# Optimization experiments

Measured on AMD Instinct MI355X. Metric: run time of the kernel, lower is better.

## Reference

```python
import jax, jax.numpy as jnp
import numpy as np

N_NODES = 100000
N_EDGES = 800000
N_GRAPHS = 64
D = 256
IN_FEAT = 59
MLP_DIMS = [D // 2, D // 2, D // 4, D // 8, 1]  # 128->128->64->32->1


def _glorot(key, shape):
    fan_in = shape[0] if len(shape) > 1 else shape[0]
    return jax.random.normal(key, shape, dtype=jnp.float32) / jnp.sqrt(jnp.float32(fan_in))


def setup_inputs() -> dict:
    key = jax.random.key(0)
    ks = list(jax.random.split(key, 40))
    inp = {}
    inp['x'] = jax.random.normal(ks[0], (N_NODES, IN_FEAT), dtype=jnp.float32)
    inp['edge_index'] = jax.random.randint(ks[1], (2, N_EDGES), 0, N_NODES, dtype=jnp.int64 if jax.config.jax_enable_x64 else jnp.int32)
    inp['batch'] = jnp.sort(jax.random.randint(ks[2], (N_NODES,), 0, N_GRAPHS, dtype=jnp.int32))
    # GATConv params (heads=1): lin weight, att_src, att_dst, bias
    dims = [(IN_FEAT, D), (D, D // 2), (D // 2, D // 2)]
    ki = 3
    for li, (di, do) in enumerate(dims, start=1):
        inp[f'W{li}'] = _glorot(ks[ki], (di, do)); ki += 1
        inp[f'as{li}'] = _glorot(ks[ki], (do,)); ki += 1
        inp[f'ad{li}'] = _glorot(ks[ki], (do,)); ki += 1
        inp[f'b{li}'] = jnp.zeros((do,), dtype=jnp.float32)
    # policy / value MLPs
    for pre in ('p', 'v'):
        for j in range(4):
            inp[f'{pre}W{j}'] = _glorot(ks[ki], (MLP_DIMS[j], MLP_DIMS[j + 1])); ki += 1
            inp[f'{pre}b{j}'] = jnp.zeros((MLP_DIMS[j + 1],), dtype=jnp.float32)
    return inp


def gat_conv(x, src, dst, W, a_src, a_dst, b, n_nodes):
    """PyG GATConv, heads=1, self-loops already included in src/dst."""
    h = x @ W  # [N, Do]
    s = h @ a_src  # [N] per-node source score
    d = h @ a_dst  # [N] per-node target score
    e = jax.nn.leaky_relu(s[src] + d[dst], negative_slope=0.2)  # [E]
    m = jax.ops.segment_max(e, dst, num_segments=n_nodes)
    m = jnp.where(jnp.isfinite(m), m, 0.0)
    ex = jnp.exp(e - m[dst])
    den = jax.ops.segment_sum(ex, dst, num_segments=n_nodes)
    alpha = ex / (den[dst] + 1e-16)  # edge softmax over incoming edges
    out = jax.ops.segment_sum(h[src] * alpha[:, None], dst, num_segments=n_nodes)
    return out + b


def mlp(h, Ws, bs):
    # hidden layers with ReLU, final layer linear
    for W, b in zip(Ws[:-1], bs[:-1]):
        h = jax.nn.relu(h @ W + b)
    return h @ Ws[-1] + bs[-1]


def reference(x, edge_index, batch,
              W1, as1, ad1, b1, W2, as2, ad2, b2, W3, as3, ad3, b3,
              pW0, pb0, pW1, pb1, pW2, pb2, pW3, pb3,
              vW0, vb0, vW1, vb1, vW2, vb2, vW3, vb3):
    n = x.shape[0]
    loop = jnp.arange(n, dtype=edge_index.dtype)
    src = jnp.concatenate([edge_index[0], loop])  # PyG adds self-loops
    dst = jnp.concatenate([edge_index[1], loop])
    out = jax.nn.relu(gat_conv(x, src, dst, W1, as1, ad1, b1, n))
    out = jax.nn.relu(gat_conv(out, src, dst, W2, as2, ad2, b2, n))
    out = jax.nn.relu(gat_conv(out, src, dst, W3, as3, ad3, b3, n))
    policy = mlp(out, [pW0, pW1, pW2, pW3], [pb0, pb1, pb2, pb3])  # [N, 1]
    pooled = jax.ops.segment_sum(out, batch, num_segments=N_GRAPHS)  # global_add_pool
    value = mlp(pooled, [vW0, vW1, vW2, vW3], [vb0, vb1, vb2, vb3])  # [G, 1]
    # Original returns policy split per-graph (data-dependent slicing); the
    # dense [N,1] policy plus batch ids carries the same information.
    return policy, value
```

## Files before the change

kernel.cpp:

```cpp
#include <hip/hip_runtime.h>
#include <hip/hip_bf16.h>
#include <cstdint>

#define N_NODES 100000
#define N_EDGES 800000
#define N_GRAPHS 64
#define POOL_SPLIT 16

typedef short short8 __attribute__((ext_vector_type(8)));
typedef float f32x4 __attribute__((ext_vector_type(4)));

__device__ __forceinline__ float leakyf(float x){ return x >= 0.0f ? x : 0.2f*x; }
__device__ __forceinline__ float reluf(float x){ return x > 0.0f ? x : 0.0f; }

__device__ __forceinline__ float bf2f(unsigned short u){
  union { uint32_t i; float f; } c; c.i = ((uint32_t)u) << 16; return c.f;
}
__device__ __forceinline__ unsigned short f2bf(float x){
  union { float f; uint32_t i; } c; c.f = x;
  uint32_t r = c.i + 0x7FFFu + ((c.i >> 16) & 1u);
  return (unsigned short)(r >> 16);
}
__device__ __forceinline__ uint32_t pack2(float a, float b){
  return (uint32_t)f2bf(a) | ((uint32_t)f2bf(b) << 16);
}

__global__ __launch_bounds__(256) void x2bf_kernel(const float* __restrict__ x,
    uint32_t* __restrict__ xb, int n){
  int idx = blockIdx.x*256 + threadIdx.x;
  if (idx >= n*32) return;
  int v = idx >> 5, c2 = (idx & 31)*2;
  float f0 = (c2   < 59) ? x[(size_t)v*59 + c2]     : 0.f;
  float f1 = (c2+1 < 59) ? x[(size_t)v*59 + c2 + 1] : 0.f;
  xb[idx] = pack2(f0, f1);
}

__global__ void zero_deg_kernel(int* __restrict__ deg, int n){
  int v = blockIdx.x*256 + threadIdx.x;
  if (v < n) deg[v] = 0;
}
__global__ void count_kernel(const int* __restrict__ dst, int* __restrict__ deg,
                             int* __restrict__ pos, int E){
  int e = blockIdx.x*256 + threadIdx.x;
  if (e < E) pos[e] = atomicAdd(&deg[dst[e]], 1);
}
__global__ __launch_bounds__(256) void scan1_kernel(const int* __restrict__ deg,
    int* __restrict__ rowptr, int* __restrict__ bsum, int n){
  __shared__ int sm[256];
  int t = threadIdx.x, i = blockIdx.x*256 + t;
  int v = (i < n) ? deg[i] : 0;
  sm[t] = v; __syncthreads();
  for (int off = 1; off < 256; off <<= 1){
    int x = (t >= off) ? sm[t-off] : 0;
    __syncthreads();
    sm[t] += x;
    __syncthreads();
  }
  if (i < n) rowptr[i] = sm[t] - v;
  if (t == 255) bsum[blockIdx.x] = sm[255];
}
__global__ __launch_bounds__(512) void scan2_kernel(int* __restrict__ bsum, int nb){
  __shared__ int sm[512];
  int t = threadIdx.x;
  int v = (t < nb) ? bsum[t] : 0;
  sm[t] = v; __syncthreads();
  for (int off = 1; off < 512; off <<= 1){
    int x = (t >= off) ? sm[t-off] : 0;
    __syncthreads();
    sm[t] += x;
    __syncthreads();
  }
  if (t < nb) bsum[t] = sm[t] - v;
}
__global__ void scan3_kernel(int* __restrict__ rowptr, const int* __restrict__ bsum, int n){
  int i = blockIdx.x*256 + threadIdx.x;
  if (i < n) rowptr[i] += bsum[blockIdx.x];
}
__global__ void scatter_kernel(const int* __restrict__ src, const int* __restrict__ dst,
                               const int* __restrict__ rowptr, const int* __restrict__ pos,
                               int* __restrict__ csr, int E){
  int e = blockIdx.x*256 + threadIdx.x;
  if (e < E) csr[rowptr[dst[e]] + pos[e]] = src[e];
}

__global__ __launch_bounds__(256) void wa_all_kernel(
    const float* __restrict__ W1, const float* __restrict__ as1, const float* __restrict__ ad1,
    const float* __restrict__ W2, const float* __restrict__ as2, const float* __restrict__ ad2,
    const float* __restrict__ W3, const float* __restrict__ as3, const float* __restrict__ ad3,
    float* __restrict__ wa){
  int t = threadIdx.x;
  { float ss=0.f, dd=0.f; const float* wr = W2 + (size_t)t*128;
    for (int o=0;o<128;++o){ float w=wr[o]; ss+=w*as2[o]; dd+=w*ad2[o]; }
    wa[128+t]=ss; wa[384+t]=dd; }
  if (t < 128){ float ss=0.f, dd=0.f; const float* wr = W3 + (size_t)t*128;
    for (int o=0;o<128;++o){ float w=wr[o]; ss+=w*as3[o]; dd+=w*ad3[o]; }
    wa[640+t]=ss; wa[768+t]=dd; }
  if (t < 64){ float ss=0.f, dd=0.f;
    if (t < 59){ const float* wr = W1 + (size_t)t*256;
      for (int o=0;o<256;++o){ float w=wr[o]; ss+=w*as1[o]; dd+=w*ad1[o]; } }
    wa[t]=ss; wa[64+t]=dd; }
}

__global__ __launch_bounds__(256) void sd_bf16_kernel(const unsigned short* __restrict__ in,
    const float* __restrict__ wa_s, const float* __restrict__ wa_d,
    float* __restrict__ s, float* __restrict__ d, int n, int K){
  int wid = threadIdx.x >> 6, lane = threadIdx.x & 63;
  int v = (blockIdx.x << 2) + wid;
  if (v >= n) return;
  float ss = 0.f, dd = 0.f;
  const unsigned short* row = in + (size_t)v*K;
  for (int k = lane*2; k < K; k += 128){
    uint32_t u = *(const uint32_t*)&row[k];
    float x0 = bf2f((unsigned short)(u & 0xFFFFu));
    float x1 = bf2f((unsigned short)(u >> 16));
    ss += x0*wa_s[k] + x1*wa_s[k+1];
    dd += x0*wa_d[k] + x1*wa_d[k+1];
  }
  for (int off = 32; off; off >>= 1){ ss += __shfl_down(ss, off); dd += __shfl_down(dd, off); }
  if (lane == 0){ s[v] = ss; d[v] = dd; }
}

template<int NC>
__device__ __forceinline__ void gload(const unsigned short* rowp, int hl, float* f){
  if constexpr (NC == 1){
    uint32_t u = ((const uint32_t*)rowp)[hl];
    f[0] = bf2f((unsigned short)(u & 0xFFFFu));
    f[1] = bf2f((unsigned short)(u >> 16));
  } else {
    uint2 u = ((const uint2*)rowp)[hl];
    f[0] = bf2f((unsigned short)(u.x & 0xFFFFu));
    f[1] = bf2f((unsigned short)(u.x >> 16));
    f[2] = bf2f((unsigned short)(u.y & 0xFFFFu));
    f[3] = bf2f((unsigned short)(u.y >> 16));
  }
}

template<int NC, int BR>
__global__ __launch_bounds__(256) void agg_half(
    const unsigned short* __restrict__ hb, const float* __restrict__ s,
    const float* __restrict__ dsc, const int* __restrict__ rowptr,
    const int* __restrict__ deg, const int* __restrict__ csr, float* __restrict__ ew,
    const float* __restrict__ bias, unsigned short* __restrict__ outp, int n){
  const int C = NC*64;
  const int tid = threadIdx.x;
  const int hl   = tid & 31;
  const int base = tid & 32;
  const int v = blockIdx.x*8 + (tid >> 5);
  if (v >= n) return;
  const int beg = rowptr[v], dg = deg[v];
  const float dv = dsc[v];
  const float e0 = leakyf(s[v] + dv);
  float acc[2*NC];

  if (dg <= 32){
    int srcl = 0; float sc = -1e30f;
    if (hl < dg){ srcl = csr[beg + hl]; sc = leakyf(s[srcl] + dv); }
    float mm = sc;
    #pragma unroll
    for (int off = 16; off; off >>= 1) mm = fmaxf(mm, __shfl_xor(mm, off));
    const float m = fmaxf(e0, mm);
    float w = (hl < dg) ? __expf(sc - m) : 0.f;
    float den = w;
    #pragma unroll
    for (int off = 16; off; off >>= 1) den += __shfl_xor(den, off);
    const float ws0 = __expf(e0 - m);
    const float inv = 1.0f / (den + ws0 + 1e-16f);
    const float wl = w * inv;
    {
      float f[2*NC]; gload<NC>(hb + (size_t)v*C, hl, f);
      const float w0 = ws0 * inv;
      #pragma unroll
      for (int c = 0; c < 2*NC; ++c) acc[c] = w0 * f[c];
    }
    int j = 0;
    for (; j + 4 <= dg; j += 4){
      int  s0 = __shfl(srcl, base+j),   s1 = __shfl(srcl, base+j+1);
      int  s2 = __shfl(srcl, base+j+2), s3 = __shfl(srcl, base+j+3);
      float w0_ = __shfl(wl, base+j),   w1_ = __shfl(wl, base+j+1);
      float w2_ = __shfl(wl, base+j+2), w3_ = __shfl(wl, base+j+3);
      float f0[2*NC], f1[2*NC], f2[2*NC], f3[2*NC];
      gload<NC>(hb + (size_t)s0*C, hl, f0);
      gload<NC>(hb + (size_t)s1*C, hl, f1);
      gload<NC>(hb + (size_t)s2*C, hl, f2);
      gload<NC>(hb + (size_t)s3*C, hl, f3);
      #pragma unroll
      for (int c = 0; c < 2*NC; ++c)
        acc[c] += w0_*f0[c] + w1_*f1[c] + w2_*f2[c] + w3_*f3[c];
    }
    for (; j < dg; ++j){
      int src = __shfl(srcl, base+j);
      float w_ = __shfl(wl, base+j);
      float f[2*NC]; gload<NC>(hb + (size_t)src*C, hl, f);
      #pragma unroll
      for (int c = 0; c < 2*NC; ++c) acc[c] += w_*f[c];
    }
  } else {
    float m = e0;
    for (int b0 = 0; b0 < dg; b0 += 32){
      int i = b0 + hl; float sc = -1e30f;
      if (i < dg){ int src = csr[beg + i]; sc = leakyf(s[src] + dv); ew[beg + i] = sc; }
      #pragma unroll
      for (int off = 16; off; off >>= 1) sc = fmaxf(sc, __shfl_xor(sc, off));
      m = fmaxf(m, sc);
    }
    float dsum = 0.f;
    for (int b0 = 0; b0 < dg; b0 += 32){
      int i = b0 + hl; float w = 0.f;
      if (i < dg){ w = __expf(ew[beg + i] - m); ew[beg + i] = w; }
      float cs = w;
      #pragma unroll
      for (int off = 16; off; off >>= 1) cs += __shfl_xor(cs, off);
      dsum += cs;
    }
    const float ws0 = __expf(e0 - m);
    const float inv = 1.0f / (dsum + ws0 + 1e-16f);
    {
      float f[2*NC]; gload<NC>(hb + (size_t)v*C, hl, f);
      const float w0 = ws0 * inv;
      #pragma unroll
      for (int c = 0; c < 2*NC; ++c) acc[c] = w0 * f[c];
    }
    for (int b0 = 0; b0 < dg; b0 += 32){
      int i = b0 + hl;
      int srcl = 0; float wl = 0.f;
      if (i < dg){ srcl = csr[beg + i]; wl = ew[beg + i] * inv; }
      int cnt = min(32, dg - b0);
      for (int j = 0; j < cnt; ++j){
        int src = __shfl(srcl, base+j);
        float w_ = __shfl(wl, base+j);
        float f[2*NC]; gload<NC>(hb + (size_t)src*C, hl, f);
        #pragma unroll
        for (int c = 0; c < 2*NC; ++c) acc[c] += w_*f[c];
      }
    }
  }

  unsigned short* op = outp + (size_t)v*C;
  if constexpr (NC == 1){
    float v0 = acc[0], v1 = acc[1];
    if constexpr (BR){ v0 = reluf(v0 + bias[2*hl]); v1 = reluf(v1 + bias[2*hl+1]); }
    ((uint32_t*)op)[hl] = pack2(v0, v1);
  } else {
    float v0=acc[0], v1=acc[1], v2=acc[2], v3=acc[3];
    if constexpr (BR){
      v0 = reluf(v0 + bias[4*hl]);   v1 = reluf(v1 + bias[4*hl+1]);
      v2 = reluf(v2 + bias[4*hl+2]); v3 = reluf(v3 + bias[4*hl+3]);
    }
    uint2 u; u.x = pack2(v0, v1); u.y = pack2(v2, v3);
    ((uint2*)op)[hl] = u;
  }
}

template<int ABF, int OBF>
__global__ __launch_bounds__(256) void gemm_mfma(
    const void* __restrict__ Av, const float* __restrict__ W,
    const float* __restrict__ bias, void* __restrict__ Cv,
    int M, int K, int Kw, int N, int act){
  __shared__ short As[64][40];
  __shared__ short Bs[64][40];
  const int t = threadIdx.x;
  const int row0 = blockIdx.x * 64;
  const int col0 = blockIdx.y * 64;
  const int wv = t >> 6, lane = t & 63;
  const int wr = wv >> 1, wc = wv & 1;
  const int lr = lane & 15, lg = lane >> 4;

  f32x4 acc00 = {}, acc01 = {}, acc10 = {}, acc11 = {};

  for (int k0 = 0; k0 < K; k0 += 32){
    {
      int m = t >> 2, kq = (t & 3) * 8;
      int gr = row0 + m;
      short8 av;
      if constexpr (ABF == 1){
        const unsigned short* Au = (const unsigned short*)Av;
        if (gr < M && (k0 + kq + 7) < K){
          av = *(const short8*)&Au[(size_t)gr*K + k0 + kq];
        } else {
          #pragma unroll
          for (int j = 0; j < 8; ++j){
            int gk = k0 + kq + j;
            av[j] = (gr < M && gk < K) ? (short)Au[(size_t)gr*K + gk] : (short)0;
          }
        }
      } else {
        const float* Af = (const float*)Av;
        if (gr < M && (K % 4) == 0 && (k0 + kq + 7) < K){
          const float4 f0 = *(const float4*)&Af[(size_t)gr*K + k0 + kq];
          const float4 f1 = *(const float4*)&Af[(size_t)gr*K + k0 + kq + 4];
          av[0]=f2bf(f0.x); av[1]=f2bf(f0.y); av[2]=f2bf(f0.z); av[3]=f2bf(f0.w);
          av[4]=f2bf(f1.x); av[5]=f2bf(f1.y); av[6]=f2bf(f1.z); av[7]=f2bf(f1.w);
        } else {
          #pragma unroll
          for (int j = 0; j < 8; ++j){
            int gk = k0 + kq + j;
            float val = (gr < M && gk < K) ? Af[(size_t)gr*K + gk] : 0.f;
            av[j] = f2bf(val);
          }
        }
      }
      *(short8*)&As[m][kq] = av;
    }
    {
      int n = t & 63, k8 = (t >> 6) * 8;
      short8 bv;
      #pragma unroll
      for (int j = 0; j < 8; ++j){
        int gk = k0 + k8 + j;
        float val = (gk < Kw) ? W[(size_t)gk*N + col0 + n] : 0.f;
        bv[j] = f2bf(val);
      }
      *(short8*)&Bs[n][k8] = bv;
    }
    __syncthreads();
    short8 af0 = *(short8*)&As[wr*32 +  0 + lr][lg*8];
    short8 af1 = *(short8*)&As[wr*32 + 16 + lr][lg*8];
    short8 bf0 = *(short8*)&Bs[wc*32 +  0 + lr][lg*8];
    short8 bf1 = *(short8*)&Bs[wc*32 + 16 + lr][lg*8];
    acc00 = __builtin_amdgcn_mfma_f32_16x16x32_bf16(af0, bf0, acc00, 0, 0, 0);
    acc01 = __builtin_amdgcn_mfma_f32_16x16x32_bf16(af0, bf1, acc01, 0, 0, 0);
    acc10 = __builtin_amdgcn_mfma_f32_16x16x32_bf16(af1, bf0, acc10, 0, 0, 0);
    acc11 = __builtin_amdgcn_mfma_f32_16x16x32_bf16(af1, bf1, acc11, 0, 0, 0);
    __syncthreads();
  }

  #pragma unroll
  for (int fm = 0; fm < 2; ++fm){
    #pragma unroll
    for (int fn = 0; fn < 2; ++fn){
      const f32x4 a = (fm==0) ? (fn==0 ? acc00 : acc01) : (fn==0 ? acc10 : acc11);
      int col = col0 + wc*32 + fn*16 + lr;
      float bv = bias ? bias[col] : 0.f;
      #pragma unroll
      for (int j = 0; j < 4; ++j){
        int row = row0 + wr*32 + fm*16 + lg*4 + j;
        if (row >= M) continue;
        float val = a[j] + bv;
        if (act) val = reluf(val);
        if constexpr (OBF == 0) ((float*)Cv)[(size_t)row*N + col] = val;
        else ((unsigned short*)Cv)[(size_t)row*N + col] = f2bf(val);
      }
    }
  }
}

__global__ __launch_bounds__(256) void policy_tail_kernel(
    const float* __restrict__ p2, const float* __restrict__ W2, const float* __restrict__ B2,
    const float* __restrict__ W3, const float* __restrict__ B3,
    float* __restrict__ out, int n){
  __shared__ float w2[64*32];
  __shared__ float w3[32];
  __shared__ float b2s[32];
  int t = threadIdx.x;
  for (int i = t; i < 2048; i += 256) w2[i] = W2[i];
  if (t < 32){ w3[t] = W3[t]; b2s[t] = B2[t]; }
  __syncthreads();
  int v = blockIdx.x*256 + t;
  if (v >= n) return;
  const float* row = p2 + (size_t)v*64;
  float acc32[32];
  #pragma unroll
  for (int o = 0; o < 32; ++o) acc32[o] = b2s[o];
  for (int k = 0; k < 64; ++k){
    float xk = row[k];
    #pragma unroll
    for (int o = 0; o < 32; ++o) acc32[o] += xk * w2[k*32 + o];
  }
  float accf = B3[0];
  #pragma unroll
  for (int o = 0; o < 32; ++o) accf += reluf(acc32[o]) * w3[o];
  out[v] = accf;
}

__global__ void bounds_kernel(const int* __restrict__ batch, int* __restrict__ gstart,
                              int n, int G){
  int g = threadIdx.x;
  if (g > G) return;
  int lo = 0, hi = n;
  while (lo < hi){ int mid = (lo + hi) >> 1; if (batch[mid] < g) lo = mid + 1; else hi = mid; }
  gstart[g] = lo;
}

__global__ __launch_bounds__(128) void pool_split_kernel(const float* __restrict__ x,
    const int* __restrict__ gstart, float* __restrict__ partial){
  int g = blockIdx.x, sp = blockIdx.y, f = threadIdx.x;
  int beg = gstart[g], end = gstart[g+1];
  int len = end - beg;
  int chunk = (len + POOL_SPLIT - 1) / POOL_SPLIT;
  int lo = beg + sp*chunk;
  int hi = min(lo + chunk, end);
  float acc = 0.f;
  for (int r = lo; r < hi; ++r) acc += x[(size_t)r*128 + f];
  partial[((size_t)g*POOL_SPLIT + sp)*128 + f] = acc;
}
__global__ __launch_bounds__(128) void pool_final_kernel(const float* __restrict__ partial,
    float* __restrict__ pooled){
  int g = blockIdx.x, f = threadIdx.x;
  float acc = 0.f;
  #pragma unroll
  for (int sp = 0; sp < POOL_SPLIT; ++sp)
    acc += partial[((size_t)g*POOL_SPLIT + sp)*128 + f];
  pooled[g*128 + f] = acc;
}

__global__ __launch_bounds__(128) void value_mlp_kernel(const float* __restrict__ pooled,
    const float* __restrict__ W0, const float* __restrict__ B0,
    const float* __restrict__ W1, const float* __restrict__ B1,
    const float* __restrict__ W2, const float* __restrict__ B2,
    const float* __restrict__ W3, const float* __restrict__ B3,
    float* __restrict__ outv){
  __shared__ float a[128], b[128];
  int g = blockIdx.x, t = threadIdx.x;
  a[t] = pooled[g*128 + t];
  __syncthreads();
  float acc = B0[t];
  for (int k = 0; k < 128; ++k) acc += a[k]*W0[k*128 + t];
  b[t] = reluf(acc);
  __syncthreads();
  if (t < 64){ acc = B1[t]; for (int k = 0; k < 128; ++k) acc += b[k]*W1[k*64 + t]; a[t] = reluf(acc); }
  __syncthreads();
  if (t < 32){ acc = B2[t]; for (int k = 0; k < 64; ++k) acc += a[k]*W2[k*32 + t]; b[t] = reluf(acc); }
  __syncthreads();
  if (t == 0){ acc = B3[0]; for (int k = 0; k < 32; ++k) acc += b[k]*W3[k]; outv[g] = acc; }
}

extern "C" void kernel_launch(void* const* d_in, const int* in_sizes, int n_in,
                              void* d_out, int out_size, void* d_ws, size_t ws_size,
                              hipStream_t stream){
  const float* x     = (const float*)d_in[0];
  const int*   ei    = (const int*)d_in[1];
  const int*   batch = (const int*)d_in[2];
  const float* W1 = (const float*)d_in[3];
  const float* as1= (const float*)d_in[4];
  const float* ad1= (const float*)d_in[5];
  const float* b1 = (const float*)d_in[6];
  const float* W2 = (const float*)d_in[7];
  const float* as2= (const float*)d_in[8];
  const float* ad2= (const float*)d_in[9];
  const float* b2 = (const float*)d_in[10];
  const float* W3 = (const float*)d_in[11];
  const float* as3= (const float*)d_in[12];
  const float* ad3= (const float*)d_in[13];
  const float* b3 = (const float*)d_in[14];
  const float* pW0= (const float*)d_in[15];
  const float* pb0= (const float*)d_in[16];
  const float* pW1= (const float*)d_in[17];
  const float* pb1= (const float*)d_in[18];
  const float* pW2= (const float*)d_in[19];
  const float* pb2= (const float*)d_in[20];
  const float* pW3= (const float*)d_in[21];
  const float* pb3= (const float*)d_in[22];
  const float* vW0= (const float*)d_in[23];
  const float* vb0= (const float*)d_in[24];
  const float* vW1= (const float*)d_in[25];
  const float* vb1= (const float*)d_in[26];
  const float* vW2= (const float*)d_in[27];
  const float* vb2= (const float*)d_in[28];
  const float* vW3= (const float*)d_in[29];
  const float* vb3= (const float*)d_in[30];
  float* out = (float*)d_out;

  char* ws = (char*)d_ws;
  size_t off = 0;
  auto carve = [&](size_t bytes)->char*{
    char* p = ws + off; off = (off + bytes + 255) & ~(size_t)255; return p;
  };
  int*   deg    = (int*)  carve((size_t)N_NODES*4);
  int*   rowptr = (int*)  carve((size_t)(N_NODES+1)*4);
  int*   pos    = (int*)  carve((size_t)N_EDGES*4);
  int*   csr    = (int*)  carve((size_t)N_EDGES*4);
  int*   bsum   = (int*)  carve(512*4);
  float* ew     = (float*)carve((size_t)N_EDGES*4);
  float* s      = (float*)carve((size_t)N_NODES*4);
  float* dsc    = (float*)carve((size_t)N_NODES*4);
  float* wa     = (float*)carve(1024*4);
  int*   gstart = (int*)  carve(65*4);
  float* pooled = (float*)carve((size_t)N_GRAPHS*128*4);
  float* partial= (float*)carve((size_t)N_GRAPHS*POOL_SPLIT*128*4);
  uint32_t*       xb   = (uint32_t*)      carve((size_t)N_NODES*64*2);
  unsigned short* aggx = (unsigned short*)carve((size_t)N_NODES*64*2);
  unsigned short* out1 = (unsigned short*)carve((size_t)N_NODES*256*2);
  unsigned short* h2   = (unsigned short*)carve((size_t)N_NODES*128*2);
  unsigned short* out2 = (unsigned short*)carve((size_t)N_NODES*128*2);
  unsigned short* agg3 = (unsigned short*)carve((size_t)N_NODES*128*2);
  float* out3 = (float*)carve((size_t)N_NODES*128*4);
  unsigned short* p1 = h2;
  float* p2 = (float*)out1;

  const int* esrc = ei;
  const int* edst = ei + N_EDGES;

  const int NBn = (N_NODES + 255)/256;
  const int NBe = (N_EDGES + 255)/256;
  const int GB  = (N_NODES + 63) / 64;
  const int NB4 = (N_NODES + 3) / 4;
  const int NB8 = (N_NODES + 7) / 8;

  x2bf_kernel<<<(N_NODES*32 + 255)/256, 256, 0, stream>>>(x, xb, N_NODES);
  zero_deg_kernel<<<NBn, 256, 0, stream>>>(deg, N_NODES);
  count_kernel<<<NBe, 256, 0, stream>>>(edst, deg, pos, N_EDGES);
  scan1_kernel<<<NBn, 256, 0, stream>>>(deg, rowptr, bsum, N_NODES);
  scan2_kernel<<<1, 512, 0, stream>>>(bsum, NBn);
  scan3_kernel<<<NBn, 256, 0, stream>>>(rowptr, bsum, N_NODES);
  scatter_kernel<<<NBe, 256, 0, stream>>>(esrc, edst, rowptr, pos, csr, N_EDGES);
  wa_all_kernel<<<1, 256, 0, stream>>>(W1, as1, ad1, W2, as2, ad2, W3, as3, ad3, wa);
  bounds_kernel<<<1, 128, 0, stream>>>(batch, gstart, N_NODES, N_GRAPHS);

  sd_bf16_kernel<<<NB4, 256, 0, stream>>>((const unsigned short*)xb, wa+0, wa+64, s, dsc, N_NODES, 64);
  agg_half<1,0><<<NB8, 256, 0, stream>>>((const unsigned short*)xb, s, dsc, rowptr, deg, csr, ew,
                                         nullptr, aggx, N_NODES);
  gemm_mfma<1,1><<<dim3(GB,4), 256, 0, stream>>>(aggx, W1, b1, out1, N_NODES, 64, 59, 256, 1);

  sd_bf16_kernel<<<NB4, 256, 0, stream>>>(out1, wa+128, wa+384, s, dsc, N_NODES, 256);
  gemm_mfma<1,1><<<dim3(GB,2), 256, 0, stream>>>(out1, W2, nullptr, h2, N_NODES, 256, 256, 128, 0);
  agg_half<2,1><<<NB8, 256, 0, stream>>>(h2, s, dsc, rowptr, deg, csr, ew, b2, out2, N_NODES);

  sd_bf16_kernel<<<NB4, 256, 0, stream>>>(out2, wa+640, wa+768, s, dsc, N_NODES, 128);
  agg_half<2,0><<<NB8, 256, 0, stream>>>(out2, s, dsc, rowptr, deg, csr, ew, nullptr, agg3, N_NODES);
  gemm_mfma<1,0><<<dim3(GB,2), 256, 0, stream>>>(agg3, W3, b3, out3, N_NODES, 128, 128, 128, 1);

  gemm_mfma<0,1><<<dim3(GB,2), 256, 0, stream>>>(out3, pW0, pb0, p1, N_NODES, 128, 128, 128, 1);
  gemm_mfma<1,0><<<dim3(GB,1), 256, 0, stream>>>(p1, pW1, pb1, p2, N_NODES, 128, 128, 64, 1);
  policy_tail_kernel<<<NBn, 256, 0, stream>>>(p2, pW2, pb2, pW3, pb3, out, N_NODES);

  pool_split_kernel<<<dim3(N_GRAPHS, POOL_SPLIT), 128, 0, stream>>>(out3, gstart, partial);
  pool_final_kernel<<<N_GRAPHS, 128, 0, stream>>>(partial, pooled);
  value_mlp_kernel<<<N_GRAPHS, 128, 0, stream>>>(pooled, vW0, vb0, vW1, vb1, vW2, vb2, vW3, vb3,
                                                 out + N_NODES);
}
```

Measured before the change: 575.0 us.

## Fuse score computation into conversion and aggregation, use 16-lane node groups

Merges the x-to-bf16 conversion with the layer-1 source/target score dot products, so one sd_bf16 launch and one re-read of xb go away. The layer-2 aggregation now also computes the layer-3 attention scores from its output while still in registers, using separate s2/d2 buffers to avoid overwriting inputs in use, which removes another sd_bf16 pass. The aggregation kernel now maps 16 lanes per node with wider 8- or 16-byte vector loads instead of 32 lanes, so each wavefront handles more nodes. The trade-off is that fewer lanes share each node's neighbours, and nodes with more than 16 in-edges fall back to the slower multi-pass path more often.

```diff
diff --git a/kernel.cpp b/kernel.cpp
--- a/kernel.cpp
+++ b/kernel.cpp
@@ -23,16 +23,6 @@
 }
 __device__ __forceinline__ uint32_t pack2(float a, float b){
   return (uint32_t)f2bf(a) | ((uint32_t)f2bf(b) << 16);
-}
-
-__global__ __launch_bounds__(256) void x2bf_kernel(const float* __restrict__ x,
-    uint32_t* __restrict__ xb, int n){
-  int idx = blockIdx.x*256 + threadIdx.x;
-  if (idx >= n*32) return;
-  int v = idx >> 5, c2 = (idx & 31)*2;
-  float f0 = (c2   < 59) ? x[(size_t)v*59 + c2]     : 0.f;
-  float f1 = (c2+1 < 59) ? x[(size_t)v*59 + c2 + 1] : 0.f;
-  xb[idx] = pack2(f0, f1);
 }
 
 __global__ void zero_deg_kernel(int* __restrict__ deg, int n){
@@ -101,6 +91,23 @@
     wa[t]=ss; wa[64+t]=dd; }
 }
 
+__global__ __launch_bounds__(256) void x2bf_sd_kernel(const float* __restrict__ x,
+    const float* __restrict__ wa_s, const float* __restrict__ wa_d,
+    uint32_t* __restrict__ xb, float* __restrict__ s, float* __restrict__ d, int n){
+  int hl = threadIdx.x & 31;
+  int v = blockIdx.x*8 + (threadIdx.x >> 5);
+  if (v >= n) return;
+  int c0 = 2*hl, c1 = 2*hl + 1;
+  float f0 = (c0 < 59) ? x[(size_t)v*59 + c0] : 0.f;
+  float f1 = (c1 < 59) ? x[(size_t)v*59 + c1] : 0.f;
+  xb[(size_t)v*32 + hl] = pack2(f0, f1);
+  float ss = f0*wa_s[c0] + f1*wa_s[c1];
+  float dd = f0*wa_d[c0] + f1*wa_d[c1];
+  #pragma unroll
+  for (int off = 16; off; off >>= 1){ ss += __shfl_xor(ss, off); dd += __shfl_xor(dd, off); }
+  if (hl == 0){ s[v] = ss; d[v] = dd; }
+}
+
 __global__ __launch_bounds__(256) void sd_bf16_kernel(const unsigned short* __restrict__ in,
     const float* __restrict__ wa_s, const float* __restrict__ wa_d,
     float* __restrict__ s, float* __restrict__ d, int n, int K){
@@ -121,56 +128,60 @@
 }
 
 template<int NC>
-__device__ __forceinline__ void gload(const unsigned short* rowp, int hl, float* f){
+__device__ __forceinline__ void qload(const unsigned short* rowp, int ql, float* f){
   if constexpr (NC == 1){
-    uint32_t u = ((const uint32_t*)rowp)[hl];
-    f[0] = bf2f((unsigned short)(u & 0xFFFFu));
-    f[1] = bf2f((unsigned short)(u >> 16));
+    uint2 u = ((const uint2*)rowp)[ql];
+    f[0]=bf2f((unsigned short)(u.x & 0xFFFFu)); f[1]=bf2f((unsigned short)(u.x >> 16));
+    f[2]=bf2f((unsigned short)(u.y & 0xFFFFu)); f[3]=bf2f((unsigned short)(u.y >> 16));
   } else {
-    uint2 u = ((const uint2*)rowp)[hl];
-    f[0] = bf2f((unsigned short)(u.x & 0xFFFFu));
-    f[1] = bf2f((unsigned short)(u.x >> 16));
-    f[2] = bf2f((unsigned short)(u.y & 0xFFFFu));
-    f[3] = bf2f((unsigned short)(u.y >> 16));
-  }
-}
-
-template<int NC, int BR>
-__global__ __launch_bounds__(256) void agg_half(
+    uint4 u = ((const uint4*)rowp)[ql];
+    f[0]=bf2f((unsigned short)(u.x & 0xFFFFu)); f[1]=bf2f((unsigned short)(u.x >> 16));
+    f[2]=bf2f((unsigned short)(u.y & 0xFFFFu)); f[3]=bf2f((unsigned short)(u.y >> 16));
+    f[4]=bf2f((unsigned short)(u.z & 0xFFFFu)); f[5]=bf2f((unsigned short)(u.z >> 16));
+    f[6]=bf2f((unsigned short)(u.w & 0xFFFFu)); f[7]=bf2f((unsigned short)(u.w >> 16));
+  }
+}
+
+template<int NC, int BR, int SDF>
+__global__ __launch_bounds__(256) void agg_q(
     const unsigned short* __restrict__ hb, const float* __restrict__ s,
     const float* __restrict__ dsc, const int* __restrict__ rowptr,
     const int* __restrict__ deg, const int* __restrict__ csr, float* __restrict__ ew,
-    const float* __restrict__ bias, unsigned short* __restrict__ outp, int n){
-  const int C = NC*64;
-  const int tid = threadIdx.x;
-  const int hl   = tid & 31;
-  const int base = tid & 32;
-  const int v = blockIdx.x*8 + (tid >> 5);
+    const float* __restrict__ bias,
+    const float* __restrict__ sdw_s, const float* __restrict__ sdw_d,
+    float* __restrict__ s_out, float* __restrict__ d_out,
+    unsigned short* __restrict__ outp, int n){
+  const int C  = NC*64;
+  const int CH = NC*4;
+  const int tid  = threadIdx.x;
+  const int ql   = tid & 15;
+  const int base = (tid & 63) & 48;
+  const int v = blockIdx.x*16 + (tid >> 4);
   if (v >= n) return;
   const int beg = rowptr[v], dg = deg[v];
   const float dv = dsc[v];
   const float e0 = leakyf(s[v] + dv);
-  float acc[2*NC];
-
-  if (dg <= 32){
+  float acc[CH];
+
+  if (dg <= 16){
     int srcl = 0; float sc = -1e30f;
-    if (hl < dg){ srcl = csr[beg + hl]; sc = leakyf(s[srcl] + dv); }
+    if (ql < dg){ srcl = csr[beg + ql]; sc = leakyf(s[srcl] + dv); }
     float mm = sc;
     #pragma unroll
-    for (int off = 16; off; off >>= 1) mm = fmaxf(mm, __shfl_xor(mm, off));
+    for (int off = 8; off; off >>= 1) mm = fmaxf(mm, __shfl_xor(mm, off));
     const float m = fmaxf(e0, mm);
-    float w = (hl < dg) ? __expf(sc - m) : 0.f;
+    float w = (ql < dg) ? __expf(sc - m) : 0.f;
     float den = w;
     #pragma unroll
-    for (int off = 16; off; off >>= 1) den += __shfl_xor(den, off);
+    for (int off = 8; off; off >>= 1) den += __shfl_xor(den, off);
     const float ws0 = __expf(e0 - m);
     const float inv = 1.0f / (den + ws0 + 1e-16f);
     const float wl = w * inv;
     {
-      float f[2*NC]; gload<NC>(hb + (size_t)v*C, hl, f);
+      float f[CH]; qload<NC>(hb + (size_t)v*C, ql, f);
       const float w0 = ws0 * inv;
       #pragma unroll
-      for (int c = 0; c < 2*NC; ++c) acc[c] = w0 * f[c];
+      for (int c = 0; c < CH; ++c) acc[c] = w0 * f[c];
     }
     int j = 0;
     for (; j + 4 <= dg; j += 4){
@@ -178,76 +189,90 @@
       int  s2 = __shfl(srcl, base+j+2), s3 = __shfl(srcl, base+j+3);
       float w0_ = __shfl(wl, base+j),   w1_ = __shfl(wl, base+j+1);
       float w2_ = __shfl(wl, base+j+2), w3_ = __shfl(wl, base+j+3);
-      float f0[2*NC], f1[2*NC], f2[2*NC], f3[2*NC];
-      gload<NC>(hb + (size_t)s0*C, hl, f0);
-      gload<NC>(hb + (size_t)s1*C, hl, f1);
-      gload<NC>(hb + (size_t)s2*C, hl, f2);
-      gload<NC>(hb + (size_t)s3*C, hl, f3);
-      #pragma unroll
-      for (int c = 0; c < 2*NC; ++c)
+      float f0[CH], f1[CH], f2[CH], f3[CH];
+      qload<NC>(hb + (size_t)s0*C, ql, f0);
+      qload<NC>(hb + (size_t)s1*C, ql, f1);
+      qload<NC>(hb + (size_t)s2*C, ql, f2);
+      qload<NC>(hb + (size_t)s3*C, ql, f3);
+      #pragma unroll
+      for (int c = 0; c < CH; ++c)
         acc[c] += w0_*f0[c] + w1_*f1[c] + w2_*f2[c] + w3_*f3[c];
     }
     for (; j < dg; ++j){
       int src = __shfl(srcl, base+j);
       float w_ = __shfl(wl, base+j);
-      float f[2*NC]; gload<NC>(hb + (size_t)src*C, hl, f);
-      #pragma unroll
-      for (int c = 0; c < 2*NC; ++c) acc[c] += w_*f[c];
+      float f[CH]; qload<NC>(hb + (size_t)src*C, ql, f);
+      #pragma unroll
+      for (int c = 0; c < CH; ++c) acc[c] += w_*f[c];
     }
   } else {
     float m = e0;
-    for (int b0 = 0; b0 < dg; b0 += 32){
-      int i = b0 + hl; float sc = -1e30f;
+    for (int b0 = 0; b0 < dg; b0 += 16){
+      int i = b0 + ql; float sc = -1e30f;
       if (i < dg){ int src = csr[beg + i]; sc = leakyf(s[src] + dv); ew[beg + i] = sc; }
       #pragma unroll
-      for (int off = 16; off; off >>= 1) sc = fmaxf(sc, __shfl_xor(sc, off));
+      for (int off = 8; off; off >>= 1) sc = fmaxf(sc, __shfl_xor(sc, off));
       m = fmaxf(m, sc);
     }
     float dsum = 0.f;
-    for (int b0 = 0; b0 < dg; b0 += 32){
-      int i = b0 + hl; float w = 0.f;
+    for (int b0 = 0; b0 < dg; b0 += 16){
+      int i = b0 + ql; float w = 0.f;
       if (i < dg){ w = __expf(ew[beg + i] - m); ew[beg + i] = w; }
       float cs = w;
       #pragma unroll
-      for (int off = 16; off; off >>= 1) cs += __shfl_xor(cs, off);
+      for (int off = 8; off; off >>= 1) cs += __shfl_xor(cs, off);
       dsum += cs;
     }
     const float ws0 = __expf(e0 - m);
     const float inv = 1.0f / (dsum + ws0 + 1e-16f);
     {
-      float f[2*NC]; gload<NC>(hb + (size_t)v*C, hl, f);
+      float f[CH]; qload<NC>(hb + (size_t)v*C, ql, f);
       const float w0 = ws0 * inv;
       #pragma unroll
-      for (int c = 0; c < 2*NC; ++c) acc[c] = w0 * f[c];
-    }
-    for (int b0 = 0; b0 < dg; b0 += 32){
-      int i = b0 + hl;
+      for (int c = 0; c < CH; ++c) acc[c] = w0 * f[c];
+    }
+    for (int b0 = 0; b0 < dg; b0 += 16){
+      int i = b0 + ql;
       int srcl = 0; float wl = 0.f;
       if (i < dg){ srcl = csr[beg + i]; wl = ew[beg + i] * inv; }
-      int cnt = min(32, dg - b0);
+      int cnt = min(16, dg - b0);
       for (int j = 0; j < cnt; ++j){
         int src = __shfl(srcl, base+j);
         float w_ = __shfl(wl, base+j);
-        float f[2*NC]; gload<NC>(hb + (size_t)src*C, hl, f);
+        float f[CH]; qload<NC>(hb + (size_t)src*C, ql, f);
         #pragma unroll
-        for (int c = 0; c < 2*NC; ++c) acc[c] += w_*f[c];
+        for (int c = 0; c < CH; ++c) acc[c] += w_*f[c];
       }
     }
   }
 
+  float vout[CH];
+  #pragma unroll
+  for (int c = 0; c < CH; ++c){
+    float val = acc[c];
+    if constexpr (BR) val = reluf(val + bias[CH*ql + c]);
+    vout[c] = val;
+  }
   unsigned short* op = outp + (size_t)v*C;
   if constexpr (NC == 1){
-    float v0 = acc[0], v1 = acc[1];
-    if constexpr (BR){ v0 = reluf(v0 + bias[2*hl]); v1 = reluf(v1 + bias[2*hl+1]); }
-    ((uint32_t*)op)[hl] = pack2(v0, v1);
+    uint2 u; u.x = pack2(vout[0], vout[1]); u.y = pack2(vout[2], vout[3]);
+    ((uint2*)op)[ql] = u;
   } else {
-    float v0=acc[0], v1=acc[1], v2=acc[2], v3=acc[3];
-    if constexpr (BR){
-      v0 = reluf(v0 + bias[4*hl]);   v1 = reluf(v1 + bias[4*hl+1]);
-      v2 = reluf(v2 + bias[4*hl+2]); v3 = reluf(v3 + bias[4*hl+3]);
-    }
-    uint2 u; u.x = pack2(v0, v1); u.y = pack2(v2, v3);
-    ((uint2*)op)[hl] = u;
+    uint4 u;
+    u.x = pack2(vout[0], vout[1]); u.y = pack2(vout[2], vout[3]);
+    u.z = pack2(vout[4], vout[5]); u.w = pack2(vout[6], vout[7]);
+    ((uint4*)op)[ql] = u;
+  }
+  if constexpr (SDF){
+    float ss = 0.f, dd = 0.f;
+    #pragma unroll
+    for (int c = 0; c < CH; ++c){
+      ss += vout[c] * sdw_s[CH*ql + c];
+      dd += vout[c] * sdw_d[CH*ql + c];
+    }
+    #pragma unroll
+    for (int off = 8; off; off >>= 1){ ss += __shfl_xor(ss, off); dd += __shfl_xor(dd, off); }
+    if (ql == 0){ s_out[v] = ss; d_out[v] = dd; }
   }
 }
 
@@ -473,6 +498,8 @@
   float* ew     = (float*)carve((size_t)N_EDGES*4);
   float* s      = (float*)carve((size_t)N_NODES*4);
   float* dsc    = (float*)carve((size_t)N_NODES*4);
+  float* s2     = (float*)carve((size_t)N_NODES*4);
+  float* d2     = (float*)carve((size_t)N_NODES*4);
   float* wa     = (float*)carve(1024*4);
   int*   gstart = (int*)  carve(65*4);
   float* pooled = (float*)carve((size_t)N_GRAPHS*128*4);
@@ -490,33 +517,36 @@
   const int* esrc = ei;
   const int* edst = ei + N_EDGES;
 
-  const int NBn = (N_NODES + 255)/256;
-  const int NBe = (N_EDGES + 255)/256;
-  const int GB  = (N_NODES + 63) / 64;
-  const int NB4 = (N_NODES + 3) / 4;
-  const int NB8 = (N_NODES + 7) / 8;
-
-  x2bf_kernel<<<(N_NODES*32 + 255)/256, 256, 0, stream>>>(x, xb, N_NODES);
+  const int NBn  = (N_NODES + 255)/256;
+  const int NBe  = (N_EDGES + 255)/256;
+  const int GB   = (N_NODES + 63) / 64;
+  const int NB4  = (N_NODES + 3) / 4;
+  const int NB8  = (N_NODES + 7) / 8;
+  const int NB16 = (N_NODES + 15) / 16;
+
+  wa_all_kernel<<<1, 256, 0, stream>>>(W1, as1, ad1, W2, as2, ad2, W3, as3, ad3, wa);
   zero_deg_kernel<<<NBn, 256, 0, stream>>>(deg, N_NODES);
   count_kernel<<<NBe, 256, 0, stream>>>(edst, deg, pos, N_EDGES);
   scan1_kernel<<<NBn, 256, 0, stream>>>(deg, rowptr, bsum, N_NODES);
   scan2_kernel<<<1, 512, 0, stream>>>(bsum, NBn);
   scan3_kernel<<<NBn, 256, 0, stream>>>(rowptr, bsum, N_NODES);
   scatter_kernel<<<NBe, 256, 0, stream>>>(esrc, edst, rowptr, pos, csr, N_EDGES);
-  wa_all_kernel<<<1, 256, 0, stream>>>(W1, as1, ad1, W2, as2, ad2, W3, as3, ad3, wa);
+  x2bf_sd_kernel<<<NB8, 256, 0, stream>>>(x, wa+0, wa+64, xb, s, dsc, N_NODES);
   bounds_kernel<<<1, 128, 0, stream>>>(batch, gstart, N_NODES, N_GRAPHS);
 
-  sd_bf16_kernel<<<NB4, 256, 0, stream>>>((const unsigned short*)xb, wa+0, wa+64, s, dsc, N_NODES, 64);
-  agg_half<1,0><<<NB8, 256, 0, stream>>>((const unsigned short*)xb, s, dsc, rowptr, deg, csr, ew,
-                                         nullptr, aggx, N_NODES);
+  agg_q<1,0,0><<<NB16, 256, 0, stream>>>((const unsigned short*)xb, s, dsc, rowptr, deg, csr, ew,
+                                         nullptr, nullptr, nullptr, nullptr, nullptr,
+                                         aggx, N_NODES);
   gemm_mfma<1,1><<<dim3(GB,4), 256, 0, stream>>>(aggx, W1, b1, out1, N_NODES, 64, 59, 256, 1);
 
   sd_bf16_kernel<<<NB4, 256, 0, stream>>>(out1, wa+128, wa+384, s, dsc, N_NODES, 256);
   gemm_mfma<1,1><<<dim3(GB,2), 256, 0, stream>>>(out1, W2, nullptr, h2, N_NODES, 256, 256, 128, 0);
-  agg_half<2,1><<<NB8, 256, 0, stream>>>(h2, s, dsc, rowptr, deg, csr, ew, b2, out2, N_NODES);
-
-  sd_bf16_kernel<<<NB4, 256, 0, stream>>>(out2, wa+640, wa+768, s, dsc, N_NODES, 128);
-  agg_half<2,0><<<NB8, 256, 0, stream>>>(out2, s, dsc, rowptr, deg, csr, ew, nullptr, agg3, N_NODES);
+  agg_q<2,1,1><<<NB16, 256, 0, stream>>>(h2, s, dsc, rowptr, deg, csr, ew,
+                                         b2, wa+640, wa+768, s2, d2, out2, N_NODES);
+
+  agg_q<2,0,0><<<NB16, 256, 0, stream>>>(out2, s2, d2, rowptr, deg, csr, ew,
+                                         nullptr, nullptr, nullptr, nullptr, nullptr,
+                                         agg3, N_NODES);
   gemm_mfma<1,0><<<dim3(GB,2), 256, 0, stream>>>(agg3, W3, b3, out3, N_NODES, 128, 128, 128, 1);
 
   gemm_mfma<0,1><<<dim3(GB,2), 256, 0, stream>>>(out3, pW0, pb0, p1, N_NODES, 128, 128, 128, 1);
```

New measurement: 556.4 us. 1.03x faster.
